# Kernel optimization log

Hardware: AMD Instinct MI355X
Metric: run time of the kernel (lower is better)

Reference implementation:

```python
import jax, jax.numpy as jnp
import numpy as np

N, K, D = 32768, 4096, 1024

def setup_inputs() -> dict:
    key = jax.random.key(0)
    kz, kk, kv = jax.random.split(key, 3)
    z = jax.random.normal(kz, (N, D), dtype=jnp.float32)
    keys = jax.random.normal(kk, (K, D), dtype=jnp.float32)
    values = jax.random.normal(kv, (K, D), dtype=jnp.float32)
    return {"z": z, "keys": keys, "values": values}

def reference(z, keys, values):
    # scores: [N, K]
    scores = jnp.einsum('nd,kd->nk', z, keys)
    attn = jax.nn.softmax(scores, axis=-1)
    return jnp.einsum('nk,kd->nd', attn, values)
```

## Files before the change

kernel.cpp:

```cpp
#include <hip/hip_runtime.h>
#include <hip/hip_bf16.h>

typedef __attribute__((ext_vector_type(8))) short bf16x8;
typedef __attribute__((ext_vector_type(4))) float f32x4;
typedef __attribute__((ext_vector_type(4))) int   i32x4;
typedef signed char i8;

#define N_ROWS 32768
#define K_KEYS 4096
#define DDIM   1024
#define BM 32
#define BK 128
#define NBLK (K_KEYS / BK)
#define SP 132
#define SC2 (1.52587890625e-05f)

__device__ __forceinline__ ushort f2bf(float f) {
    __hip_bfloat16 b = __float2bfloat16(f);
    return *(ushort*)&b;
}
__device__ __forceinline__ float bf2f(ushort u) {
    __hip_bfloat16 b = *(__hip_bfloat16*)&u;
    return __bfloat162float(b);
}
__device__ __forceinline__ int clampi(int x) { return x > 127 ? 127 : (x < -127 ? -127 : x); }

__device__ __forceinline__ int pidx(int r, int c_us) { return r * 128 + (c_us ^ ((r & 7) << 3)); }

__device__ __forceinline__ void barrier_lgkm() {
    asm volatile("s_waitcnt lgkmcnt(0)" ::: "memory");
    __builtin_amdgcn_s_barrier();
    asm volatile("" ::: "memory");
}

__global__ void prep_kb(const float* __restrict__ keys, i8* __restrict__ sb) {
    int idx  = blockIdx.x * 256 + threadIdx.x;
    int lane = idx & 63, tile = idx >> 6;
    int g = tile >> 5, m = tile & 31;
    int key = g * 16 + (lane & 15);
    int d0  = m * 32 + (lane >> 4) * 8;
    const float* s = keys + (size_t)key * DDIM + d0;
    union { i32x4 v; i8 b[16]; } u;
#pragma unroll
    for (int e = 0; e < 8; e++) {
        float q = s[e];
        int h = clampi((int)rintf(q * 16.f));
        int l = clampi((int)rintf((q - (float)h * 0.0625f) * 4096.f));
        u.b[2 * e]     = (i8)l;
        u.b[2 * e + 1] = (i8)h;
    }
    *(i32x4*)(sb + (size_t)tile * 1024 + lane * 16) = u.v;
}

__global__ void prep_vt(const float* __restrict__ v, ushort* __restrict__ vt) {
    __shared__ float t[32][33];
    const int tk = blockIdx.x;
    const int td = blockIdx.y;
    const int tx = threadIdx.x & 31;
    const int ty = threadIdx.x >> 5;
#pragma unroll
    for (int r = 0; r < 4; r++) {
        int k = tk * 32 + ty + 8 * r;
        t[ty + 8 * r][tx] = v[(size_t)k * DDIM + td * 32 + tx];
    }
    __syncthreads();
    if (threadIdx.x < 128) {
        int s    = threadIdx.x >> 6;
        int lane = threadIdx.x & 63;
        int l16  = lane & 15, lq = lane >> 4;
        int dg   = td * 2 + s;
        int dl   = s * 16 + l16;
        bf16x8 o;
#pragma unroll
        for (int e = 0; e < 8; e++)
            o[e] = (short)f2bf(t[lq * 8 + e][dl]);
        *(bf16x8*)(vt + ((size_t)dg * 128 + tk) * 512 + lane * 8) = o;
    }
}

__launch_bounds__(512, 2)
__global__ void attn_main(const float* __restrict__ z,
                          const i8* __restrict__ sb,
                          const ushort* __restrict__ vtp,
                          float* __restrict__ out) {
    __shared__ unsigned Sx[BM][SP];
    __shared__ ushort Pt2[2][BM * 128];
    __shared__ float  m_s[BM], l_s[BM], sc_s[BM];

    const int tid  = threadIdx.x;
    const int wave = tid >> 6;
    const int lane = tid & 63;
    const int l16  = lane & 15;
    const int lq   = lane >> 4;
    const int row0 = blockIdx.x * BM;

    i32x4 qM2[2][4], qP1z[2][4];
#pragma unroll
    for (int rg = 0; rg < 2; rg++) {
        int row = row0 + rg * 16 + l16;
        const float* zr = z + (size_t)row * DDIM + wave * 128;
#pragma unroll
        for (int m = 0; m < 4; m++) {
            union { i32x4 v; i8 b[16]; } u, w;
            const float* s = zr + m * 32 + lq * 8;
#pragma unroll
            for (int e = 0; e < 8; e++) {
                float q = s[e];
                int h = clampi((int)rintf(q * 16.f));
                int l = clampi((int)rintf((q - (float)h * 0.0625f) * 4096.f));
                u.b[2 * e]     = (i8)h;
                u.b[2 * e + 1] = (i8)l;
                w.b[2 * e]     = 0;
                w.b[2 * e + 1] = (i8)h;
            }
            qM2[rg][m]  = u.v;
            qP1z[rg][m] = w.v;
        }
    }
    if (tid < BM) { m_s[tid] = -1e30f; l_s[tid] = 0.f; }
    for (int i = tid; i < BM * SP; i += 512)
        ((unsigned*)Sx)[i] = 0u;
    __syncthreads();

    f32x4 Oacc[2][8];
#pragma unroll
    for (int mt = 0; mt < 2; mt++)
#pragma unroll
        for (int nt = 0; nt < 8; nt++)
            Oacc[mt][nt] = (f32x4){0.f, 0.f, 0.f, 0.f};

    const i8* sbB = sb + (size_t)wave * 4096 + lane * 16;
    const ushort* vtB = vtp + (size_t)wave * 524288 + lane * 8;

    i32x4 kB[2][4];
#define LOADKB(gg, buf)                                                        \
    do {                                                                       \
        const i8* _b = sbB + (size_t)(gg) * 32768;                             \
        kB[buf][0] = *(const i32x4*)_b;                                        \
        kB[buf][1] = *(const i32x4*)(_b + 1024);                               \
        kB[buf][2] = *(const i32x4*)(_b + 2048);                               \
        kB[buf][3] = *(const i32x4*)(_b + 3072);                               \
    } while (0)

    LOADKB(0, 0);

    for (int b = 0; b < NBLK; b++) {
#pragma unroll
        for (int gt = 0; gt < 8; gt++) {
            const int cb = gt & 1, nb2 = cb ^ 1;
            if (gt < 7) {
                LOADKB(8 * b + gt + 1, nb2);
            } else {
                int gn = (b + 1 < NBLK) ? 8 * (b + 1) : 8 * b;
                LOADKB(gn, nb2);
            }
            i32x4 p1a = {0,0,0,0}, p1b = {0,0,0,0};
            i32x4 m2ae = {0,0,0,0}, m2ao = {0,0,0,0};
            i32x4 m2be = {0,0,0,0}, m2bo = {0,0,0,0};
            m2ae = __builtin_amdgcn_mfma_i32_16x16x64_i8(qM2[0][0],  kB[cb][0], m2ae, 0, 0, 0);
            m2be = __builtin_amdgcn_mfma_i32_16x16x64_i8(qM2[1][0],  kB[cb][0], m2be, 0, 0, 0);
            p1a  = __builtin_amdgcn_mfma_i32_16x16x64_i8(qP1z[0][0], kB[cb][0], p1a,  0, 0, 0);
            p1b  = __builtin_amdgcn_mfma_i32_16x16x64_i8(qP1z[1][0], kB[cb][0], p1b,  0, 0, 0);
            m2ao = __builtin_amdgcn_mfma_i32_16x16x64_i8(qM2[0][1],  kB[cb][1], m2ao, 0, 0, 0);
            m2bo = __builtin_amdgcn_mfma_i32_16x16x64_i8(qM2[1][1],  kB[cb][1], m2bo, 0, 0, 0);
            p1a  = __builtin_amdgcn_mfma_i32_16x16x64_i8(qP1z[0][1], kB[cb][1], p1a,  0, 0, 0);
            p1b  = __builtin_amdgcn_mfma_i32_16x16x64_i8(qP1z[1][1], kB[cb][1], p1b,  0, 0, 0);
            m2ae = __builtin_amdgcn_mfma_i32_16x16x64_i8(qM2[0][2],  kB[cb][2], m2ae, 0, 0, 0);
            m2be = __builtin_amdgcn_mfma_i32_16x16x64_i8(qM2[1][2],  kB[cb][2], m2be, 0, 0, 0);
            p1a  = __builtin_amdgcn_mfma_i32_16x16x64_i8(qP1z[0][2], kB[cb][2], p1a,  0, 0, 0);
            p1b  = __builtin_amdgcn_mfma_i32_16x16x64_i8(qP1z[1][2], kB[cb][2], p1b,  0, 0, 0);
            m2ao = __builtin_amdgcn_mfma_i32_16x16x64_i8(qM2[0][3],  kB[cb][3], m2ao, 0, 0, 0);
            m2bo = __builtin_amdgcn_mfma_i32_16x16x64_i8(qM2[1][3],  kB[cb][3], m2bo, 0, 0, 0);
            p1a  = __builtin_amdgcn_mfma_i32_16x16x64_i8(qP1z[0][3], kB[cb][3], p1a,  0, 0, 0);
            p1b  = __builtin_amdgcn_mfma_i32_16x16x64_i8(qP1z[1][3], kB[cb][3], p1b,  0, 0, 0);

            const int col = gt * 16 + l16;
#pragma unroll
            for (int r = 0; r < 4; r++) {
                int fa = p1a[r] * 256 + m2ae[r] + m2ao[r];
                int fb = p1b[r] * 256 + m2be[r] + m2bo[r];
                atomicAdd(&Sx[lq * 4 + r][col],      (unsigned)fa);
                atomicAdd(&Sx[16 + lq * 4 + r][col], (unsigned)fb);
            }
        }

        bf16x8 vbuf[2][8];
        const ushort* vtI = vtB + (size_t)b * 2048;
#pragma unroll
        for (int nt = 0; nt < 8; nt++)
            vbuf[0][nt] = *(const bf16x8*)(vtI + nt * 65536);

        barrier_lgkm();

        {
            const int row = tid >> 4;
            const int c0  = tid & 15;
            i32x4 w0 = *(const i32x4*)&Sx[row][8 * c0];
            i32x4 w1 = *(const i32x4*)&Sx[row][8 * c0 + 4];
            *(i32x4*)&Sx[row][8 * c0]     = (i32x4){0,0,0,0};
            *(i32x4*)&Sx[row][8 * c0 + 4] = (i32x4){0,0,0,0};
            float sv[8];
#pragma unroll
            for (int j = 0; j < 4; j++) {
                sv[j]     = (float)w0[j] * SC2;
                sv[4 + j] = (float)w1[j] * SC2;
            }
            float mloc = sv[0];
#pragma unroll
            for (int j = 1; j < 8; j++) mloc = fmaxf(mloc, sv[j]);
#pragma unroll
            for (int off = 8; off >= 1; off >>= 1)
                mloc = fmaxf(mloc, __shfl_xor(mloc, off));
            float m_old = m_s[row];
            float m_new = fmaxf(m_old, mloc);
            float psum = 0.f;
            bf16x8 pb;
#pragma unroll
            for (int j = 0; j < 8; j++) {
                float p = __expf(sv[j] - m_new);
                psum += p;
                pb[j] = (short)f2bf(p);
            }
            *(bf16x8*)&Pt2[b & 1][pidx(row, 8 * c0)] = pb;
#pragma unroll
            for (int off = 8; off >= 1; off >>= 1)
                psum += __shfl_xor(psum, off);
            if (c0 == 0) {
                float sc = __expf(m_old - m_new);
                l_s[row] = l_s[row] * sc + psum;
                m_s[row] = m_new;
                sc_s[row] = sc;
            }
        }
        barrier_lgkm();

        float sc0[4], sc1[4];
#pragma unroll
        for (int r = 0; r < 4; r++) {
            sc0[r] = sc_s[lq * 4 + r];
            sc1[r] = sc_s[16 + lq * 4 + r];
        }
#pragma unroll
        for (int nt = 0; nt < 8; nt++)
#pragma unroll
            for (int r = 0; r < 4; r++) {
                Oacc[0][nt][r] *= sc0[r];
                Oacc[1][nt][r] *= sc1[r];
            }

        const ushort* PtC = &Pt2[b & 1][0];
#pragma unroll
        for (int kc = 0; kc < 4; kc++) {
            if (kc < 3) {
#pragma unroll
                for (int nt = 0; nt < 8; nt++)
                    vbuf[(kc + 1) & 1][nt] = *(const bf16x8*)(vtI + nt * 65536 + (kc + 1) * 512);
            }
            bf16x8 pa0 = *(const bf16x8*)&PtC[pidx(l16, kc * 32 + lq * 8)];
            bf16x8 pa1 = *(const bf16x8*)&PtC[pidx(16 + l16, kc * 32 + lq * 8)];
#pragma unroll
            for (int nt = 0; nt < 8; nt++) {
                Oacc[0][nt] = __builtin_amdgcn_mfma_f32_16x16x32_bf16(pa0, vbuf[kc & 1][nt], Oacc[0][nt], 0, 0, 0);
                Oacc[1][nt] = __builtin_amdgcn_mfma_f32_16x16x32_bf16(pa1, vbuf[kc & 1][nt], Oacc[1][nt], 0, 0, 0);
            }
        }
    }
    __syncthreads();

    float li0[4], li1[4];
#pragma unroll
    for (int r = 0; r < 4; r++) {
        li0[r] = 1.f / l_s[lq * 4 + r];
        li1[r] = 1.f / l_s[16 + lq * 4 + r];
    }
#pragma unroll
    for (int nt = 0; nt < 8; nt++) {
#pragma unroll
        for (int r = 0; r < 4; r++) {
            int col = wave * 128 + nt * 16 + l16;
            int rowA = row0 + lq * 4 + r;
            out[(size_t)rowA * DDIM + col]        = Oacc[0][nt][r] * li0[r];
            out[(size_t)(rowA + 16) * DDIM + col] = Oacc[1][nt][r] * li1[r];
        }
    }
}

extern "C" void kernel_launch(void* const* d_in, const int* in_sizes, int n_in,
                              void* d_out, int out_size, void* d_ws, size_t ws_size,
                              hipStream_t stream) {
    const float* z    = (const float*)d_in[0];
    const float* keys = (const float*)d_in[1];
    const float* vals = (const float*)d_in[2];
    float* outp = (float*)d_out;

    i8* sb = (i8*)d_ws;
    ushort* vtw = (ushort*)(sb + (size_t)8 * 1024 * 1024);

    prep_kb<<<2048, 256, 0, stream>>>(keys, sb);
    prep_vt<<<dim3(K_KEYS / 32, DDIM / 32), 256, 0, stream>>>(vals, vtw);
    attn_main<<<N_ROWS / BM, 512, 0, stream>>>(z, sb, vtw, outp);
}
```

Baseline: 1.077 ms.

## Software-pipeline PV MFMA of previous block into next block's QK loop

Restructures the main loop so the P·V bf16 MFMAs for block b-1 run interleaved with the int8 QK score MFMAs of block b, with V loads staggered across the gt iterations. The rescale factors and P tiles are double-buffered in shared memory, and an epilogue handles the final block. The aim is to overlap the two matmul phases and hide V load latency behind score computation instead of running them serially between barriers. In exchange, register pressure rises because V buffers are live across the score loop, and the prologue and epilogue add extra code.

```diff
diff --git a/kernel.cpp b/kernel.cpp
--- a/kernel.cpp
+++ b/kernel.cpp
@@ -85,7 +85,8 @@
                           float* __restrict__ out) {
     __shared__ unsigned Sx[BM][SP];
     __shared__ ushort Pt2[2][BM * 128];
-    __shared__ float  m_s[BM], l_s[BM], sc_s[BM];
+    __shared__ float  m_s[BM], l_s[BM];
+    __shared__ float  sc2[2][BM];
 
     const int tid  = threadIdx.x;
     const int wave = tid >> 6;
@@ -117,9 +118,10 @@
             qP1z[rg][m] = w.v;
         }
     }
-    if (tid < BM) { m_s[tid] = -1e30f; l_s[tid] = 0.f; }
+    if (tid < BM) { m_s[tid] = -1e30f; l_s[tid] = 0.f; sc2[1][tid] = 1.f; }
     for (int i = tid; i < BM * SP; i += 512)
         ((unsigned*)Sx)[i] = 0u;
+    *(bf16x8*)&Pt2[1][tid * 8] = (bf16x8){0,0,0,0,0,0,0,0};
     __syncthreads();
 
     f32x4 Oacc[2][8];
@@ -144,7 +146,36 @@
 
     LOADKB(0, 0);
 
+    bf16x8 vbuf[2][8];
+#pragma unroll
+    for (int nt = 0; nt < 8; nt++) {
+        vbuf[0][nt] = *(const bf16x8*)(vtB + nt * 65536);
+        vbuf[1][nt] = *(const bf16x8*)(vtB + nt * 65536 + 512);
+    }
+
     for (int b = 0; b < NBLK; b++) {
+        const int prev = (b + 1) & 1;
+        const int bp   = (b == 0) ? 0 : b - 1;
+        const ushort* vtP = vtB + (size_t)bp * 2048;
+        const ushort* vtN = vtB + (size_t)b * 2048;
+        const ushort* PtC = &Pt2[prev][0];
+
+        {
+            float sc0[4], sc1[4];
+#pragma unroll
+            for (int r = 0; r < 4; r++) {
+                sc0[r] = sc2[prev][lq * 4 + r];
+                sc1[r] = sc2[prev][16 + lq * 4 + r];
+            }
+#pragma unroll
+            for (int nt = 0; nt < 8; nt++)
+#pragma unroll
+                for (int r = 0; r < 4; r++) {
+                    Oacc[0][nt][r] *= sc0[r];
+                    Oacc[1][nt][r] *= sc1[r];
+                }
+        }
+
 #pragma unroll
         for (int gt = 0; gt < 8; gt++) {
             const int cb = gt & 1, nb2 = cb ^ 1;
@@ -174,6 +205,31 @@
             p1a  = __builtin_amdgcn_mfma_i32_16x16x64_i8(qP1z[0][3], kB[cb][3], p1a,  0, 0, 0);
             p1b  = __builtin_amdgcn_mfma_i32_16x16x64_i8(qP1z[1][3], kB[cb][3], p1b,  0, 0, 0);
 
+            {
+                const int kc = gt >> 1, rg = gt & 1, cv = kc & 1;
+                bf16x8 pa = *(const bf16x8*)&PtC[pidx(rg * 16 + l16, kc * 32 + lq * 8)];
+#pragma unroll
+                for (int nt = 0; nt < 8; nt++)
+                    Oacc[rg][nt] = __builtin_amdgcn_mfma_f32_16x16x32_bf16(pa, vbuf[cv][nt], Oacc[rg][nt], 0, 0, 0);
+            }
+            if (gt == 1) {
+#pragma unroll
+                for (int nt = 0; nt < 8; nt++)
+                    vbuf[0][nt] = *(const bf16x8*)(vtP + nt * 65536 + 2 * 512);
+            } else if (gt == 3) {
+#pragma unroll
+                for (int nt = 0; nt < 8; nt++)
+                    vbuf[1][nt] = *(const bf16x8*)(vtP + nt * 65536 + 3 * 512);
+            } else if (gt == 5) {
+#pragma unroll
+                for (int nt = 0; nt < 8; nt++)
+                    vbuf[0][nt] = *(const bf16x8*)(vtN + nt * 65536);
+            } else if (gt == 7) {
+#pragma unroll
+                for (int nt = 0; nt < 8; nt++)
+                    vbuf[1][nt] = *(const bf16x8*)(vtN + nt * 65536 + 512);
+            }
+
             const int col = gt * 16 + l16;
 #pragma unroll
             for (int r = 0; r < 4; r++) {
@@ -183,12 +239,6 @@
                 atomicAdd(&Sx[16 + lq * 4 + r][col], (unsigned)fb);
             }
         }
-
-        bf16x8 vbuf[2][8];
-        const ushort* vtI = vtB + (size_t)b * 2048;
-#pragma unroll
-        for (int nt = 0; nt < 8; nt++)
-            vbuf[0][nt] = *(const bf16x8*)(vtI + nt * 65536);
 
         barrier_lgkm();
 
@@ -229,16 +279,21 @@
                 float sc = __expf(m_old - m_new);
                 l_s[row] = l_s[row] * sc + psum;
                 m_s[row] = m_new;
-                sc_s[row] = sc;
+                sc2[b & 1][row] = sc;
             }
         }
         barrier_lgkm();
-
+    }
+
+    {
+        const int prev = (NBLK - 1) & 1;
+        const ushort* vtI = vtB + (size_t)(NBLK - 1) * 2048;
+        const ushort* PtC = &Pt2[prev][0];
         float sc0[4], sc1[4];
 #pragma unroll
         for (int r = 0; r < 4; r++) {
-            sc0[r] = sc_s[lq * 4 + r];
-            sc1[r] = sc_s[16 + lq * 4 + r];
+            sc0[r] = sc2[prev][lq * 4 + r];
+            sc1[r] = sc2[prev][16 + lq * 4 + r];
         }
 #pragma unroll
         for (int nt = 0; nt < 8; nt++)
@@ -247,25 +302,23 @@
                 Oacc[0][nt][r] *= sc0[r];
                 Oacc[1][nt][r] *= sc1[r];
             }
-
-        const ushort* PtC = &Pt2[b & 1][0];
 #pragma unroll
         for (int kc = 0; kc < 4; kc++) {
-            if (kc < 3) {
-#pragma unroll
-                for (int nt = 0; nt < 8; nt++)
-                    vbuf[(kc + 1) & 1][nt] = *(const bf16x8*)(vtI + nt * 65536 + (kc + 1) * 512);
-            }
+            const int cv = kc & 1;
             bf16x8 pa0 = *(const bf16x8*)&PtC[pidx(l16, kc * 32 + lq * 8)];
             bf16x8 pa1 = *(const bf16x8*)&PtC[pidx(16 + l16, kc * 32 + lq * 8)];
 #pragma unroll
             for (int nt = 0; nt < 8; nt++) {
-                Oacc[0][nt] = __builtin_amdgcn_mfma_f32_16x16x32_bf16(pa0, vbuf[kc & 1][nt], Oacc[0][nt], 0, 0, 0);
-                Oacc[1][nt] = __builtin_amdgcn_mfma_f32_16x16x32_bf16(pa1, vbuf[kc & 1][nt], Oacc[1][nt], 0, 0, 0);
-            }
-        }
-    }
-    __syncthreads();
+                Oacc[0][nt] = __builtin_amdgcn_mfma_f32_16x16x32_bf16(pa0, vbuf[cv][nt], Oacc[0][nt], 0, 0, 0);
+                Oacc[1][nt] = __builtin_amdgcn_mfma_f32_16x16x32_bf16(pa1, vbuf[cv][nt], Oacc[1][nt], 0, 0, 0);
+            }
+            if (kc < 2) {
+#pragma unroll
+                for (int nt = 0; nt < 8; nt++)
+                    vbuf[cv][nt] = *(const bf16x8*)(vtI + nt * 65536 + (kc + 2) * 512);
+            }
+        }
+    }
 
     float li0[4], li1[4];
 #pragma unroll
```

After: 1.909 ms. +77.2%, slower.

## Split attention block across 16 waves with 64-wide D slices

Applied to the files above, without the earlier changes.

Doubles the block to 1024 threads so each of 16 waves handles a 64-column slice of D for both the QK score partials and the PV accumulation, halving per-wave registers and MFMA work. The softmax stage is remapped to 32 threads per row with 4 columns each. This trades more atomic contention on the shared score tile and larger barriers for more waves in flight to hide latency. The launch bound changes from (512,2) to 1024, which alters register budget and occupancy.

```diff
diff --git a/kernel.cpp b/kernel.cpp
--- a/kernel.cpp
+++ b/kernel.cpp
@@ -78,7 +78,7 @@
     }
 }
 
-__launch_bounds__(512, 2)
+__launch_bounds__(1024)
 __global__ void attn_main(const float* __restrict__ z,
                           const i8* __restrict__ sb,
                           const ushort* __restrict__ vtp,
@@ -94,13 +94,13 @@
     const int lq   = lane >> 4;
     const int row0 = blockIdx.x * BM;
 
-    i32x4 qM2[2][4], qP1z[2][4];
+    i32x4 qM2[2][2], qP1z[2][2];
 #pragma unroll
     for (int rg = 0; rg < 2; rg++) {
         int row = row0 + rg * 16 + l16;
-        const float* zr = z + (size_t)row * DDIM + wave * 128;
-#pragma unroll
-        for (int m = 0; m < 4; m++) {
+        const float* zr = z + (size_t)row * DDIM + wave * 64;
+#pragma unroll
+        for (int m = 0; m < 2; m++) {
             union { i32x4 v; i8 b[16]; } u, w;
             const float* s = zr + m * 32 + lq * 8;
 #pragma unroll
@@ -118,28 +118,26 @@
         }
     }
     if (tid < BM) { m_s[tid] = -1e30f; l_s[tid] = 0.f; }
-    for (int i = tid; i < BM * SP; i += 512)
+    for (int i = tid; i < BM * SP; i += 1024)
         ((unsigned*)Sx)[i] = 0u;
     __syncthreads();
 
-    f32x4 Oacc[2][8];
+    f32x4 Oacc[2][4];
 #pragma unroll
     for (int mt = 0; mt < 2; mt++)
 #pragma unroll
-        for (int nt = 0; nt < 8; nt++)
+        for (int nt = 0; nt < 4; nt++)
             Oacc[mt][nt] = (f32x4){0.f, 0.f, 0.f, 0.f};
 
-    const i8* sbB = sb + (size_t)wave * 4096 + lane * 16;
-    const ushort* vtB = vtp + (size_t)wave * 524288 + lane * 8;
-
-    i32x4 kB[2][4];
+    const i8* sbB = sb + (size_t)wave * 2048 + lane * 16;
+    const ushort* vtB = vtp + (size_t)wave * 262144 + lane * 8;
+
+    i32x4 kB[2][2];
 #define LOADKB(gg, buf)                                                        \
     do {                                                                       \
         const i8* _b = sbB + (size_t)(gg) * 32768;                             \
         kB[buf][0] = *(const i32x4*)_b;                                        \
         kB[buf][1] = *(const i32x4*)(_b + 1024);                               \
-        kB[buf][2] = *(const i32x4*)(_b + 2048);                               \
-        kB[buf][3] = *(const i32x4*)(_b + 3072);                               \
     } while (0)
 
     LOADKB(0, 0);
@@ -155,75 +153,60 @@
                 LOADKB(gn, nb2);
             }
             i32x4 p1a = {0,0,0,0}, p1b = {0,0,0,0};
-            i32x4 m2ae = {0,0,0,0}, m2ao = {0,0,0,0};
-            i32x4 m2be = {0,0,0,0}, m2bo = {0,0,0,0};
-            m2ae = __builtin_amdgcn_mfma_i32_16x16x64_i8(qM2[0][0],  kB[cb][0], m2ae, 0, 0, 0);
-            m2be = __builtin_amdgcn_mfma_i32_16x16x64_i8(qM2[1][0],  kB[cb][0], m2be, 0, 0, 0);
-            p1a  = __builtin_amdgcn_mfma_i32_16x16x64_i8(qP1z[0][0], kB[cb][0], p1a,  0, 0, 0);
-            p1b  = __builtin_amdgcn_mfma_i32_16x16x64_i8(qP1z[1][0], kB[cb][0], p1b,  0, 0, 0);
-            m2ao = __builtin_amdgcn_mfma_i32_16x16x64_i8(qM2[0][1],  kB[cb][1], m2ao, 0, 0, 0);
-            m2bo = __builtin_amdgcn_mfma_i32_16x16x64_i8(qM2[1][1],  kB[cb][1], m2bo, 0, 0, 0);
-            p1a  = __builtin_amdgcn_mfma_i32_16x16x64_i8(qP1z[0][1], kB[cb][1], p1a,  0, 0, 0);
-            p1b  = __builtin_amdgcn_mfma_i32_16x16x64_i8(qP1z[1][1], kB[cb][1], p1b,  0, 0, 0);
-            m2ae = __builtin_amdgcn_mfma_i32_16x16x64_i8(qM2[0][2],  kB[cb][2], m2ae, 0, 0, 0);
-            m2be = __builtin_amdgcn_mfma_i32_16x16x64_i8(qM2[1][2],  kB[cb][2], m2be, 0, 0, 0);
-            p1a  = __builtin_amdgcn_mfma_i32_16x16x64_i8(qP1z[0][2], kB[cb][2], p1a,  0, 0, 0);
-            p1b  = __builtin_amdgcn_mfma_i32_16x16x64_i8(qP1z[1][2], kB[cb][2], p1b,  0, 0, 0);
-            m2ao = __builtin_amdgcn_mfma_i32_16x16x64_i8(qM2[0][3],  kB[cb][3], m2ao, 0, 0, 0);
-            m2bo = __builtin_amdgcn_mfma_i32_16x16x64_i8(qM2[1][3],  kB[cb][3], m2bo, 0, 0, 0);
-            p1a  = __builtin_amdgcn_mfma_i32_16x16x64_i8(qP1z[0][3], kB[cb][3], p1a,  0, 0, 0);
-            p1b  = __builtin_amdgcn_mfma_i32_16x16x64_i8(qP1z[1][3], kB[cb][3], p1b,  0, 0, 0);
+            i32x4 m2a = {0,0,0,0}, m2b = {0,0,0,0};
+            m2a = __builtin_amdgcn_mfma_i32_16x16x64_i8(qM2[0][0],  kB[cb][0], m2a, 0, 0, 0);
+            m2b = __builtin_amdgcn_mfma_i32_16x16x64_i8(qM2[1][0],  kB[cb][0], m2b, 0, 0, 0);
+            p1a = __builtin_amdgcn_mfma_i32_16x16x64_i8(qP1z[0][0], kB[cb][0], p1a, 0, 0, 0);
+            p1b = __builtin_amdgcn_mfma_i32_16x16x64_i8(qP1z[1][0], kB[cb][0], p1b, 0, 0, 0);
+            m2a = __builtin_amdgcn_mfma_i32_16x16x64_i8(qM2[0][1],  kB[cb][1], m2a, 0, 0, 0);
+            m2b = __builtin_amdgcn_mfma_i32_16x16x64_i8(qM2[1][1],  kB[cb][1], m2b, 0, 0, 0);
+            p1a = __builtin_amdgcn_mfma_i32_16x16x64_i8(qP1z[0][1], kB[cb][1], p1a, 0, 0, 0);
+            p1b = __builtin_amdgcn_mfma_i32_16x16x64_i8(qP1z[1][1], kB[cb][1], p1b, 0, 0, 0);
 
             const int col = gt * 16 + l16;
 #pragma unroll
             for (int r = 0; r < 4; r++) {
-                int fa = p1a[r] * 256 + m2ae[r] + m2ao[r];
-                int fb = p1b[r] * 256 + m2be[r] + m2bo[r];
+                int fa = p1a[r] * 256 + m2a[r];
+                int fb = p1b[r] * 256 + m2b[r];
                 atomicAdd(&Sx[lq * 4 + r][col],      (unsigned)fa);
                 atomicAdd(&Sx[16 + lq * 4 + r][col], (unsigned)fb);
             }
         }
 
-        bf16x8 vbuf[2][8];
+        bf16x8 vbuf[2][4];
         const ushort* vtI = vtB + (size_t)b * 2048;
 #pragma unroll
-        for (int nt = 0; nt < 8; nt++)
+        for (int nt = 0; nt < 4; nt++)
             vbuf[0][nt] = *(const bf16x8*)(vtI + nt * 65536);
 
         barrier_lgkm();
 
         {
-            const int row = tid >> 4;
-            const int c0  = tid & 15;
-            i32x4 w0 = *(const i32x4*)&Sx[row][8 * c0];
-            i32x4 w1 = *(const i32x4*)&Sx[row][8 * c0 + 4];
-            *(i32x4*)&Sx[row][8 * c0]     = (i32x4){0,0,0,0};
-            *(i32x4*)&Sx[row][8 * c0 + 4] = (i32x4){0,0,0,0};
-            float sv[8];
-#pragma unroll
-            for (int j = 0; j < 4; j++) {
-                sv[j]     = (float)w0[j] * SC2;
-                sv[4 + j] = (float)w1[j] * SC2;
-            }
-            float mloc = sv[0];
-#pragma unroll
-            for (int j = 1; j < 8; j++) mloc = fmaxf(mloc, sv[j]);
-#pragma unroll
-            for (int off = 8; off >= 1; off >>= 1)
+            const int row = tid >> 5;
+            const int c0  = tid & 31;
+            i32x4 w0 = *(const i32x4*)&Sx[row][4 * c0];
+            *(i32x4*)&Sx[row][4 * c0] = (i32x4){0,0,0,0};
+            float sv[4];
+#pragma unroll
+            for (int j = 0; j < 4; j++)
+                sv[j] = (float)w0[j] * SC2;
+            float mloc = fmaxf(fmaxf(sv[0], sv[1]), fmaxf(sv[2], sv[3]));
+#pragma unroll
+            for (int off = 16; off >= 1; off >>= 1)
                 mloc = fmaxf(mloc, __shfl_xor(mloc, off));
             float m_old = m_s[row];
             float m_new = fmaxf(m_old, mloc);
             float psum = 0.f;
-            bf16x8 pb;
-#pragma unroll
-            for (int j = 0; j < 8; j++) {
+            ushort pb[4];
+#pragma unroll
+            for (int j = 0; j < 4; j++) {
                 float p = __expf(sv[j] - m_new);
                 psum += p;
-                pb[j] = (short)f2bf(p);
-            }
-            *(bf16x8*)&Pt2[b & 1][pidx(row, 8 * c0)] = pb;
-#pragma unroll
-            for (int off = 8; off >= 1; off >>= 1)
+                pb[j] = f2bf(p);
+            }
+            *(ushort4*)&Pt2[b & 1][pidx(row, 4 * c0)] = make_ushort4(pb[0], pb[1], pb[2], pb[3]);
+#pragma unroll
+            for (int off = 16; off >= 1; off >>= 1)
                 psum += __shfl_xor(psum, off);
             if (c0 == 0) {
                 float sc = __expf(m_old - m_new);
@@ -234,32 +217,34 @@
         }
         barrier_lgkm();
 
-        float sc0[4], sc1[4];
-#pragma unroll
-        for (int r = 0; r < 4; r++) {
-            sc0[r] = sc_s[lq * 4 + r];
-            sc1[r] = sc_s[16 + lq * 4 + r];
-        }
-#pragma unroll
-        for (int nt = 0; nt < 8; nt++)
+        {
+            float sc0[4], sc1[4];
 #pragma unroll
             for (int r = 0; r < 4; r++) {
-                Oacc[0][nt][r] *= sc0[r];
-                Oacc[1][nt][r] *= sc1[r];
-            }
+                sc0[r] = sc_s[lq * 4 + r];
+                sc1[r] = sc_s[16 + lq * 4 + r];
+            }
+#pragma unroll
+            for (int nt = 0; nt < 4; nt++)
+#pragma unroll
+                for (int r = 0; r < 4; r++) {
+                    Oacc[0][nt][r] *= sc0[r];
+                    Oacc[1][nt][r] *= sc1[r];
+                }
+        }
 
         const ushort* PtC = &Pt2[b & 1][0];
 #pragma unroll
         for (int kc = 0; kc < 4; kc++) {
             if (kc < 3) {
 #pragma unroll
-                for (int nt = 0; nt < 8; nt++)
+                for (int nt = 0; nt < 4; nt++)
                     vbuf[(kc + 1) & 1][nt] = *(const bf16x8*)(vtI + nt * 65536 + (kc + 1) * 512);
             }
             bf16x8 pa0 = *(const bf16x8*)&PtC[pidx(l16, kc * 32 + lq * 8)];
             bf16x8 pa1 = *(const bf16x8*)&PtC[pidx(16 + l16, kc * 32 + lq * 8)];
 #pragma unroll
-            for (int nt = 0; nt < 8; nt++) {
+            for (int nt = 0; nt < 4; nt++) {
                 Oacc[0][nt] = __builtin_amdgcn_mfma_f32_16x16x32_bf16(pa0, vbuf[kc & 1][nt], Oacc[0][nt], 0, 0, 0);
                 Oacc[1][nt] = __builtin_amdgcn_mfma_f32_16x16x32_bf16(pa1, vbuf[kc & 1][nt], Oacc[1][nt], 0, 0, 0);
             }
@@ -274,10 +259,10 @@
         li1[r] = 1.f / l_s[16 + lq * 4 + r];
     }
 #pragma unroll
-    for (int nt = 0; nt < 8; nt++) {
+    for (int nt = 0; nt < 4; nt++) {
 #pragma unroll
         for (int r = 0; r < 4; r++) {
-            int col = wave * 128 + nt * 16 + l16;
+            int col = wave * 64 + nt * 16 + l16;
             int rowA = row0 + lq * 4 + r;
             out[(size_t)rowA * DDIM + col]        = Oacc[0][nt][r] * li0[r];
             out[(size_t)(rowA + 16) * DDIM + col] = Oacc[1][nt][r] * li1[r];
@@ -298,5 +283,5 @@
 
     prep_kb<<<2048, 256, 0, stream>>>(keys, sb);
     prep_vt<<<dim3(K_KEYS / 32, DDIM / 32), 256, 0, stream>>>(vals, vtw);
-    attn_main<<<N_ROWS / BM, 512, 0, stream>>>(z, sb, vtw, outp);
-}
+    attn_main<<<N_ROWS / BM, 1024, 0, stream>>>(z, sb, vtw, outp);
+}
```

Measured after the change: 1.070 ms. No clear change (-0.7%).
